# Performance work log

Hardware: AMD Instinct MI355X
Metric: run time of the kernel (lower is better)

## Reference

```python
import jax, jax.numpy as jnp
import numpy as np

N, E, IN, ED, H, C, G, NC = 50000, 800000, 128, 32, 4, 16, 64, 2
HC = H * C  # 64
NEG_SLOPE = 0.2
EPS = 1e-5


def _layernorm(x, g, b):
    mu = jnp.mean(x, axis=-1, keepdims=True)
    var = jnp.mean((x - mu) ** 2, axis=-1, keepdims=True)
    return (x - mu) * jax.lax.rsqrt(var + EPS) * g + b


def _gat(x, src, dst, edge_attr, W, a_src, a_dst, We, a_edge, b):
    """PyG GATConv (v1) with edge features, concat=True."""
    n = x.shape[0]
    h, c = a_src.shape
    xw = (x @ W).reshape(n, h, c)                       # [N,H,C]
    al_src = jnp.sum(xw * a_src, axis=-1)               # [N,H]
    al_dst = jnp.sum(xw * a_dst, axis=-1)               # [N,H]
    ew = (edge_attr @ We).reshape(-1, h, c)             # [Ef,H,C]
    al_e = jnp.sum(ew * a_edge, axis=-1)                # [Ef,H]
    alpha = al_src[src] + al_dst[dst] + al_e            # [Ef,H]
    alpha = jnp.where(alpha > 0, alpha, NEG_SLOPE * alpha)
    # segment softmax over incoming edges of each dst node
    amax = jax.ops.segment_max(alpha, dst, num_segments=n)
    amax = jnp.where(jnp.isfinite(amax), amax, 0.0)
    ex = jnp.exp(alpha - amax[dst])
    denom = jax.ops.segment_sum(ex, dst, num_segments=n)
    att = ex / (denom[dst] + 1e-16)                     # [Ef,H]
    msg = xw[src] * att[:, :, None]                     # [Ef,H,C]
    out = jax.ops.segment_sum(msg, dst, num_segments=n) # [N,H,C]
    return out.reshape(n, h * c) + b


def setup_inputs() -> dict:
    ks = jax.random.split(jax.random.key(0), 24)
    s = 0.1
    inp = {
        "x": jax.random.normal(ks[0], (N, IN), jnp.float32),
        "edge_attr": jax.random.normal(ks[1], (E, ED), jnp.float32),
        "W1": jax.random.normal(ks[2], (IN, HC), jnp.float32) * s,
        "as1": jax.random.normal(ks[3], (H, C), jnp.float32) * s,
        "ad1": jax.random.normal(ks[4], (H, C), jnp.float32) * s,
        "We1": jax.random.normal(ks[5], (ED, HC), jnp.float32) * s,
        "ae1": jax.random.normal(ks[6], (H, C), jnp.float32) * s,
        "b1": jnp.zeros((HC,), jnp.float32),
        "W2": jax.random.normal(ks[7], (HC, HC), jnp.float32) * s,
        "as2": jax.random.normal(ks[8], (H, C), jnp.float32) * s,
        "ad2": jax.random.normal(ks[9], (H, C), jnp.float32) * s,
        "We2": jax.random.normal(ks[10], (ED, HC), jnp.float32) * s,
        "ae2": jax.random.normal(ks[11], (H, C), jnp.float32) * s,
        "b2": jnp.zeros((HC,), jnp.float32),
        "g1": jnp.ones((HC,), jnp.float32),
        "be1": jnp.zeros((HC,), jnp.float32),
        "fw1": jax.random.normal(ks[12], (HC, 32), jnp.float32) * s,
        "fb1": jnp.zeros((32,), jnp.float32),
        "g2": jnp.ones((32,), jnp.float32),
        "be2": jnp.zeros((32,), jnp.float32),
        "fw2": jax.random.normal(ks[13], (32, NC), jnp.float32) * s,
        "fb2": jnp.zeros((NC,), jnp.float32),
        "edge_index": jax.random.randint(ks[14], (2, E), 0, N, jnp.int64),
        "batch": jnp.sort(jax.random.randint(ks[15], (N,), 0, G, jnp.int64)),
    }
    return inp


def reference(x, edge_attr, W1, as1, ad1, We1, ae1, b1, W2, as2, ad2, We2, ae2,
              b2, g1, be1, fw1, fb1, g2, be2, fw2, fb2, edge_index, batch):
    src, dst = edge_index[0], edge_index[1]
    e = edge_attr.shape[0]
    # add_self_loops with fill_value='mean' (mean of incoming edge_attr per node)
    cnt = jax.ops.segment_sum(jnp.ones((e,), x.dtype), dst, num_segments=N)
    loop_ea = jax.ops.segment_sum(edge_attr, dst, num_segments=N) / jnp.clip(cnt, 1.0)[:, None]
    ar = jnp.arange(N)
    src_f = jnp.concatenate([src, ar])
    dst_f = jnp.concatenate([dst, ar])
    ea_f = jnp.concatenate([edge_attr, loop_ea], axis=0)

    h = _gat(x, src_f, dst_f, ea_f, W1, as1, ad1, We1, ae1, b1)
    h = jax.nn.relu(h)
    h = _layernorm(h, g1, be1)
    h = _gat(h, src_f, dst_f, ea_f, W2, as2, ad2, We2, ae2, b2)
    h = jax.nn.relu(h)
    pooled = jax.ops.segment_max(h, batch, num_segments=G)   # global_max_pool
    pooled = jnp.where(jnp.isfinite(pooled), pooled, 0.0)
    z = pooled @ fw1 + fb1
    z = _layernorm(z, g2, be2)
    z = jax.nn.relu(z)
    # dropout(p=0.4) is identity in eval mode
    z = z @ fw2 + fb2
    return jax.nn.log_softmax(z, axis=1)
```

## Files before the change

### kernel.cpp

```cpp
#include <hip/hip_runtime.h>
#include <math.h>

#define N_NODES 50000
#define N_EDGES 800000
#define IN_DIM 128
#define ED_DIM 32
#define NH 4
#define CH 16
#define HC 64
#define NG 64
#define NCL 2
#define NEG_SLOPE 0.2f
#define LN_EPS 1e-5f
#define NBLK1 196

__global__ void k_ve(const float* __restrict__ We1, const float* __restrict__ ae1,
                     const float* __restrict__ We2, const float* __restrict__ ae2,
                     float* __restrict__ Ve) {
    int t = threadIdx.x;
    int d = t >> 3, k = t & 7;
    int l = k >> 2, h = k & 3;
    const float* We = l ? We2 : We1;
    const float* ae = l ? ae2 : ae1;
    float s = 0.f;
    #pragma unroll
    for (int c = 0; c < CH; ++c) s += We[d * HC + h * CH + c] * ae[h * CH + c];
    Ve[d * 8 + k] = s;
}

__global__ void k_hist(const int* __restrict__ dst, int* __restrict__ cnt,
                       int* __restrict__ rank_e) {
    int e = blockIdx.x * 256 + threadIdx.x;
    if (e < N_EDGES) rank_e[e] = atomicAdd(&cnt[dst[e]], 1);
}

__global__ void k_scan_local(const int* __restrict__ cnt, int* __restrict__ tmp_ex,
                             int* __restrict__ bsum) {
    __shared__ int sd[256];
    int t = threadIdx.x, idx = blockIdx.x * 256 + t;
    int v = (idx < N_NODES) ? cnt[idx] : 0;
    sd[t] = v; __syncthreads();
    for (int off = 1; off < 256; off <<= 1) {
        int add = (t >= off) ? sd[t - off] : 0;
        __syncthreads();
        sd[t] += add;
        __syncthreads();
    }
    if (idx < N_NODES) tmp_ex[idx] = sd[t] - v;
    if (t == 255) bsum[blockIdx.x] = sd[t];
}

__global__ void k_scan_bsums(const int* __restrict__ bsum, int* __restrict__ boff) {
    __shared__ int sd[256];
    int t = threadIdx.x;
    int v = (t < NBLK1) ? bsum[t] : 0;
    sd[t] = v; __syncthreads();
    for (int off = 1; off < 256; off <<= 1) {
        int add = (t >= off) ? sd[t - off] : 0;
        __syncthreads();
        sd[t] += add;
        __syncthreads();
    }
    boff[t] = sd[t] - v;
}

__global__ void k_scan_final(const int* __restrict__ tmp_ex, const int* __restrict__ boff,
                             int* __restrict__ row_start) {
    int idx = blockIdx.x * 256 + threadIdx.x;
    if (idx < N_NODES) row_start[idx] = tmp_ex[idx] + boff[blockIdx.x];
    if (idx == 0) row_start[N_NODES] = N_EDGES;
}

__global__ void k_perm(const int* __restrict__ dst, const int* __restrict__ rank_e,
                       const int* __restrict__ row_start, int* __restrict__ perm_csr) {
    int e = blockIdx.x * 256 + threadIdx.x;
    if (e >= N_EDGES) return;
    int pos = row_start[dst[e]] + rank_e[e];
    perm_csr[pos] = e;
}

__global__ void k_edge(const float* __restrict__ ea, const float* __restrict__ Ve,
                       float* __restrict__ ale8) {
    __shared__ float sVe[ED_DIM * 8];
    int t = threadIdx.x;
    if (t < ED_DIM * 8) sVe[t] = Ve[t];
    __syncthreads();
    int e = blockIdx.x * 256 + t;
    if (e >= N_EDGES) return;
    float a[8];
    #pragma unroll
    for (int k = 0; k < 8; ++k) a[k] = 0.f;
    const float4* er4 = (const float4*)(ea + (long long)e * ED_DIM);
    #pragma unroll
    for (int q = 0; q < ED_DIM / 4; ++q) {
        float4 v = er4[q];
        float ev[4] = {v.x, v.y, v.z, v.w};
        #pragma unroll
        for (int u = 0; u < 4; ++u) {
            #pragma unroll
            for (int k = 0; k < 8; ++k) a[k] += ev[u] * sVe[(q * 4 + u) * 8 + k];
        }
    }
    float4* ap = (float4*)(ale8 + (long long)e * 8);
    ap[0] = make_float4(a[0], a[1], a[2], a[3]);
    ap[1] = make_float4(a[4], a[5], a[6], a[7]);
}

__global__ void k_gather(const int* __restrict__ perm, const int* __restrict__ srcI,
                         const float* __restrict__ ale8, int* __restrict__ src_csr,
                         float4* __restrict__ ale1, float4* __restrict__ ale2) {
    int i = blockIdx.x * 256 + threadIdx.x;
    if (i >= N_EDGES) return;
    int e = perm[i];
    const float4* a = (const float4*)(ale8 + (long long)e * 8);
    float4 a0 = a[0];
    float4 a1 = a[1];
    src_csr[i] = srcI[e];
    ale1[i] = a0;
    ale2[i] = a1;
}

template<int K>
__global__ void k_xw(const float* __restrict__ X, const float* __restrict__ W,
                     const float* __restrict__ AS, const float* __restrict__ AD,
                     float* __restrict__ XW, float* __restrict__ ALS, float* __restrict__ ALD) {
    __shared__ float sW[K * HC];
    __shared__ float sX[16 * K];
    int t = threadIdx.x;
    for (int i = t; i < K * HC; i += 256) sW[i] = W[i];
    int nb = blockIdx.x * 16;
    for (int i = t; i < 16 * K; i += 256) sX[i] = X[(long long)nb * K + i];
    __syncthreads();
    int sub = t >> 6, j = t & 63;
    float acc[4] = {0.f, 0.f, 0.f, 0.f};
    #pragma unroll 8
    for (int k = 0; k < K; ++k) {
        float wv = sW[k * HC + j];
        #pragma unroll
        for (int q = 0; q < 4; ++q) acc[q] += sX[(sub + 4 * q) * K + k] * wv;
    }
    float as_ = AS[j], ad_ = AD[j];
    #pragma unroll
    for (int q = 0; q < 4; ++q) {
        int n = nb + sub + 4 * q;
        XW[(long long)n * HC + j] = acc[q];
        float vs = acc[q] * as_, vd = acc[q] * ad_;
        #pragma unroll
        for (int m = 1; m < 16; m <<= 1) { vs += __shfl_xor(vs, m); vd += __shfl_xor(vd, m); }
        if ((j & 15) == 0) {
            int h = j >> 4;
            ALS[n * 4 + h] = vs; ALD[n * 4 + h] = vd;
        }
    }
}

template<bool DO_LN>
__global__ void k_agg(const int* __restrict__ rs, const int* __restrict__ srcs,
                      const float* __restrict__ ale,
                      const float* __restrict__ ALS, const float* __restrict__ ALD,
                      const float* __restrict__ XW, const float* __restrict__ bias,
                      const float* __restrict__ gam, const float* __restrict__ bet,
                      float* __restrict__ OUT) {
    int n = (blockIdx.x * blockDim.x + threadIdx.x) >> 6;
    if (n >= N_NODES) return;
    int lane = threadIdx.x & 63;
    int h = lane >> 4;
    int e0 = rs[n], e1 = rs[n + 1];
    float adn = ALD[n * 4 + h];
    float acc0 = 0.f, l0 = 0.f, as0 = 0.f;
    float acc1 = 0.f, l1 = 0.f, as1 = 0.f;
    float acc2 = 0.f, l2 = 0.f, as2 = 0.f;
    float acc3 = 0.f, l3 = 0.f, as3 = 0.f;
    int e = e0;
    for (; e + 3 < e1; e += 4) {
        int sA = srcs[e], sB = srcs[e + 1], sC = srcs[e + 2], sD = srcs[e + 3];
        float aeA = ale[(e) * 4 + h];
        float aeB = ale[(e + 1) * 4 + h];
        float aeC = ale[(e + 2) * 4 + h];
        float aeD = ale[(e + 3) * 4 + h];
        float xA = XW[sA * HC + lane];
        float xB = XW[sB * HC + lane];
        float xC = XW[sC * HC + lane];
        float xD = XW[sD * HC + lane];
        float aA = ALS[sA * 4 + h] + adn + aeA;
        float aB = ALS[sB * 4 + h] + adn + aeB;
        float aC = ALS[sC * 4 + h] + adn + aeC;
        float aD = ALS[sD * 4 + h] + adn + aeD;
        aA = aA > 0.f ? aA : NEG_SLOPE * aA;
        aB = aB > 0.f ? aB : NEG_SLOPE * aB;
        aC = aC > 0.f ? aC : NEG_SLOPE * aC;
        aD = aD > 0.f ? aD : NEG_SLOPE * aD;
        float qA = __expf(aA), qB = __expf(aB), qC = __expf(aC), qD = __expf(aD);
        acc0 += qA * xA; l0 += qA; as0 += aeA;
        acc1 += qB * xB; l1 += qB; as1 += aeB;
        acc2 += qC * xC; l2 += qC; as2 += aeC;
        acc3 += qD * xD; l3 += qD; as3 += aeD;
    }
    for (; e < e1; ++e) {
        int sA = srcs[e];
        float aeA = ale[(e) * 4 + h];
        float xA = XW[sA * HC + lane];
        float aA = ALS[sA * 4 + h] + adn + aeA;
        aA = aA > 0.f ? aA : NEG_SLOPE * aA;
        float qA = __expf(aA);
        acc0 += qA * xA; l0 += qA; as0 += aeA;
    }
    int d = e1 - e0;
    float invd = 1.f / (float)(d > 0 ? d : 1);
    float aSelf = ALS[n * 4 + h] + adn + (as0 + as1 + as2 + as3) * invd;
    aSelf = aSelf > 0.f ? aSelf : NEG_SLOPE * aSelf;
    float pS = __expf(aSelf);
    float acc = (acc0 + acc1) + (acc2 + acc3) + pS * XW[n * HC + lane];
    float l = (l0 + l1) + (l2 + l3) + pS;
    float v = acc / (l + 1e-16f) + bias[lane];
    v = fmaxf(v, 0.f);
    if (DO_LN) {
        float s1 = v;
        #pragma unroll
        for (int mm = 1; mm < 64; mm <<= 1) s1 += __shfl_xor(s1, mm);
        float mean = s1 * (1.f / 64.f);
        float dd = v - mean;
        float s2 = dd * dd;
        #pragma unroll
        for (int mm = 1; mm < 64; mm <<= 1) s2 += __shfl_xor(s2, mm);
        float var = s2 * (1.f / 64.f);
        v = dd * rsqrtf(var + LN_EPS) * gam[lane] + bet[lane];
    }
    OUT[(long long)n * HC + lane] = v;
}

__global__ void k_pool(const float* __restrict__ H2, const int* __restrict__ batch,
                       float* __restrict__ pooled) {
    int j = threadIdx.x & 63;
    int r = threadIdx.x >> 6;
    int base = blockIdx.x * 128;
    int gcur = -1; float rm = 0.f;
    for (int n = base + r; n < base + 128 && n < N_NODES; n += 4) {
        int g = batch[n];
        if (g != gcur) {
            if (gcur >= 0) atomicMax((unsigned int*)&pooled[gcur * HC + j], __float_as_uint(rm));
            gcur = g; rm = 0.f;
        }
        rm = fmaxf(rm, H2[(long long)n * HC + j]);
    }
    if (gcur >= 0) atomicMax((unsigned int*)&pooled[gcur * HC + j], __float_as_uint(rm));
}

__global__ void k_head(const float* __restrict__ pooled,
                       const float* __restrict__ fw1, const float* __restrict__ fb1,
                       const float* __restrict__ g2, const float* __restrict__ be2,
                       const float* __restrict__ fw2, const float* __restrict__ fb2,
                       float* __restrict__ out) {
    int g = blockIdx.x;
    int j = threadIdx.x;
    float z = 0.f;
    if (j < 32) {
        for (int k = 0; k < HC; ++k) z += pooled[g * HC + k] * fw1[k * 32 + j];
        z += fb1[j];
    }
    float s1 = (j < 32) ? z : 0.f;
    for (int m = 1; m < 32; m <<= 1) s1 += __shfl_xor(s1, m, 32);
    float mean = s1 * (1.f / 32.f);
    float d = z - mean;
    float s2 = (j < 32) ? d * d : 0.f;
    for (int m = 1; m < 32; m <<= 1) s2 += __shfl_xor(s2, m, 32);
    float var = s2 * (1.f / 32.f);
    float zz = 0.f;
    if (j < 32) {
        zz = d * rsqrtf(var + LN_EPS) * g2[j] + be2[j];
        zz = fmaxf(zz, 0.f);
    }
    float p0 = (j < 32) ? zz * fw2[j * NCL + 0] : 0.f;
    float p1 = (j < 32) ? zz * fw2[j * NCL + 1] : 0.f;
    for (int m = 1; m < 32; m <<= 1) { p0 += __shfl_xor(p0, m, 32); p1 += __shfl_xor(p1, m, 32); }
    if (j == 0) {
        float l0 = p0 + fb2[0], l1 = p1 + fb2[1];
        float mx = fmaxf(l0, l1);
        float ls = mx + logf(__expf(l0 - mx) + __expf(l1 - mx));
        out[g * NCL + 0] = l0 - ls;
        out[g * NCL + 1] = l1 - ls;
    }
}

extern "C" void kernel_launch(void* const* d_in, const int* in_sizes, int n_in,
                              void* d_out, int out_size, void* d_ws, size_t ws_size,
                              hipStream_t stream) {
    const float* x   = (const float*)d_in[0];
    const float* ea  = (const float*)d_in[1];
    const float* W1  = (const float*)d_in[2];
    const float* as1 = (const float*)d_in[3];
    const float* ad1 = (const float*)d_in[4];
    const float* We1 = (const float*)d_in[5];
    const float* ae1 = (const float*)d_in[6];
    const float* b1  = (const float*)d_in[7];
    const float* W2  = (const float*)d_in[8];
    const float* as2 = (const float*)d_in[9];
    const float* ad2 = (const float*)d_in[10];
    const float* We2 = (const float*)d_in[11];
    const float* ae2 = (const float*)d_in[12];
    const float* b2  = (const float*)d_in[13];
    const float* g1  = (const float*)d_in[14];
    const float* be1 = (const float*)d_in[15];
    const float* fw1 = (const float*)d_in[16];
    const float* fb1 = (const float*)d_in[17];
    const float* g2  = (const float*)d_in[18];
    const float* be2 = (const float*)d_in[19];
    const float* fw2 = (const float*)d_in[20];
    const float* fb2 = (const float*)d_in[21];
    const int* eidx  = (const int*)d_in[22];
    const int* batch = (const int*)d_in[23];
    const int* srcI = eidx;
    const int* dstI = eidx + N_EDGES;

    char* w = (char*)d_ws;
    auto alloc = [&](size_t bytes) { char* p = w; w += (bytes + 255) & ~(size_t)255; return p; };
    int*   cnt       = (int*)  alloc((size_t)N_NODES * 4);
    int*   row_start = (int*)  alloc((size_t)(N_NODES + 1) * 4);
    int*   rank_e    = (int*)  alloc((size_t)N_EDGES * 4);
    int*   tmp_ex    = (int*)  alloc((size_t)N_NODES * 4);
    int*   bsum      = (int*)  alloc(256 * 4);
    int*   boff      = (int*)  alloc(256 * 4);
    float* Ve        = (float*)alloc(ED_DIM * 8 * 4);
    int*   perm_csr  = (int*)  alloc((size_t)N_EDGES * 4);
    int*   src_csr   = (int*)  alloc((size_t)N_EDGES * 4);
    float* ale8      = (float*)alloc((size_t)N_EDGES * 8 * 4);
    float4* ale1     = (float4*)alloc((size_t)N_EDGES * 16);
    float4* ale2     = (float4*)alloc((size_t)N_EDGES * 16);
    float* xw1       = (float*)alloc((size_t)N_NODES * HC * 4);
    float* als1      = (float*)alloc((size_t)N_NODES * 4 * 4);
    float* ald1      = (float*)alloc((size_t)N_NODES * 4 * 4);
    float* h1        = (float*)alloc((size_t)N_NODES * HC * 4);
    float* als2      = (float*)alloc((size_t)N_NODES * 4 * 4);
    float* ald2      = (float*)alloc((size_t)N_NODES * 4 * 4);
    float* pooled    = (float*)alloc((size_t)NG * HC * 4);
    float* xw2 = xw1;
    float* h2  = h1;

    hipMemsetAsync(cnt, 0, (size_t)N_NODES * 4, stream);
    hipMemsetAsync(pooled, 0, (size_t)NG * HC * 4, stream);

    k_ve<<<1, 256, 0, stream>>>(We1, ae1, We2, ae2, Ve);
    k_hist<<<N_EDGES / 256, 256, 0, stream>>>(dstI, cnt, rank_e);
    k_scan_local<<<NBLK1, 256, 0, stream>>>(cnt, tmp_ex, bsum);
    k_scan_bsums<<<1, 256, 0, stream>>>(bsum, boff);
    k_scan_final<<<NBLK1, 256, 0, stream>>>(tmp_ex, boff, row_start);
    k_edge<<<N_EDGES / 256, 256, 0, stream>>>(ea, Ve, ale8);
    k_perm<<<N_EDGES / 256, 256, 0, stream>>>(dstI, rank_e, row_start, perm_csr);
    k_gather<<<N_EDGES / 256, 256, 0, stream>>>(perm_csr, srcI, ale8, src_csr, ale1, ale2);

    k_xw<IN_DIM><<<N_NODES / 16, 256, 0, stream>>>(x, W1, as1, ad1, xw1, als1, ald1);
    k_agg<true><<<N_NODES / 4, 256, 0, stream>>>(row_start, src_csr, (const float*)ale1,
                                                 als1, ald1, xw1, b1, g1, be1, h1);
    k_xw<HC><<<N_NODES / 16, 256, 0, stream>>>(h1, W2, as2, ad2, xw2, als2, ald2);
    k_agg<false><<<N_NODES / 4, 256, 0, stream>>>(row_start, src_csr, (const float*)ale2,
                                                  als2, ald2, xw2, b2, nullptr, nullptr, h2);

    k_pool<<<(N_NODES + 127) / 128, 256, 0, stream>>>(h2, batch, pooled);
    k_head<<<NG, 64, 0, stream>>>(pooled, fw1, fb1, g2, be2, fw2, fb2, (float*)d_out);
}
```

Baseline: 466.4 us.

## Fuse edge projection, CSR permutation and gather into one scatter kernel

Folds the per-layer edge attention vector computation into the edge kernel's prologue, which every block now recomputes. Merges the block-sum scan into the final scan kernel by having each block redo the small 196-entry scan. Replaces the perm/ale8/gather sequence with a direct scatter of src index and edge logits to their CSR position. This removes five launches and the ale8/perm_csr intermediate traffic, at the cost of scattered (uncoalesced) writes and redundant per-block recomputation.

Result: no change. 465.1 us (-0.3%).

```diff
diff --git a/kernel.cpp b/kernel.cpp
--- a/kernel.cpp
+++ b/kernel.cpp
@@ -14,20 +14,6 @@
 #define LN_EPS 1e-5f
 #define NBLK1 196
 
-__global__ void k_ve(const float* __restrict__ We1, const float* __restrict__ ae1,
-                     const float* __restrict__ We2, const float* __restrict__ ae2,
-                     float* __restrict__ Ve) {
-    int t = threadIdx.x;
-    int d = t >> 3, k = t & 7;
-    int l = k >> 2, h = k & 3;
-    const float* We = l ? We2 : We1;
-    const float* ae = l ? ae2 : ae1;
-    float s = 0.f;
-    #pragma unroll
-    for (int c = 0; c < CH; ++c) s += We[d * HC + h * CH + c] * ae[h * CH + c];
-    Ve[d * 8 + k] = s;
-}
-
 __global__ void k_hist(const int* __restrict__ dst, int* __restrict__ cnt,
                        int* __restrict__ rank_e) {
     int e = blockIdx.x * 256 + threadIdx.x;
@@ -50,7 +36,8 @@
     if (t == 255) bsum[blockIdx.x] = sd[t];
 }
 
-__global__ void k_scan_bsums(const int* __restrict__ bsum, int* __restrict__ boff) {
+__global__ void k_scan_final(const int* __restrict__ tmp_ex, const int* __restrict__ bsum,
+                             int* __restrict__ row_start) {
     __shared__ int sd[256];
     int t = threadIdx.x;
     int v = (t < NBLK1) ? bsum[t] : 0;
@@ -61,29 +48,31 @@
         sd[t] += add;
         __syncthreads();
     }
-    boff[t] = sd[t] - v;
-}
-
-__global__ void k_scan_final(const int* __restrict__ tmp_ex, const int* __restrict__ boff,
-                             int* __restrict__ row_start) {
-    int idx = blockIdx.x * 256 + threadIdx.x;
-    if (idx < N_NODES) row_start[idx] = tmp_ex[idx] + boff[blockIdx.x];
+    int boff = sd[blockIdx.x] - bsum[blockIdx.x];
+    int idx = blockIdx.x * 256 + t;
+    if (idx < N_NODES) row_start[idx] = tmp_ex[idx] + boff;
     if (idx == 0) row_start[N_NODES] = N_EDGES;
 }
 
-__global__ void k_perm(const int* __restrict__ dst, const int* __restrict__ rank_e,
-                       const int* __restrict__ row_start, int* __restrict__ perm_csr) {
-    int e = blockIdx.x * 256 + threadIdx.x;
-    if (e >= N_EDGES) return;
-    int pos = row_start[dst[e]] + rank_e[e];
-    perm_csr[pos] = e;
-}
-
-__global__ void k_edge(const float* __restrict__ ea, const float* __restrict__ Ve,
-                       float* __restrict__ ale8) {
+__global__ void k_edge_fused(const float* __restrict__ ea,
+                             const float* __restrict__ We1, const float* __restrict__ ae1,
+                             const float* __restrict__ We2, const float* __restrict__ ae2,
+                             const int* __restrict__ dstI, const int* __restrict__ srcI,
+                             const int* __restrict__ rank_e, const int* __restrict__ row_start,
+                             float4* __restrict__ ale1, float4* __restrict__ ale2,
+                             int* __restrict__ src_csr) {
     __shared__ float sVe[ED_DIM * 8];
     int t = threadIdx.x;
-    if (t < ED_DIM * 8) sVe[t] = Ve[t];
+    {
+        int d = t >> 3, k = t & 7;
+        int l = k >> 2, h = k & 3;
+        const float* We = l ? We2 : We1;
+        const float* ae = l ? ae2 : ae1;
+        float s = 0.f;
+        #pragma unroll
+        for (int c = 0; c < CH; ++c) s += We[d * HC + h * CH + c] * ae[h * CH + c];
+        sVe[d * 8 + k] = s;
+    }
     __syncthreads();
     int e = blockIdx.x * 256 + t;
     if (e >= N_EDGES) return;
@@ -101,23 +90,10 @@
             for (int k = 0; k < 8; ++k) a[k] += ev[u] * sVe[(q * 4 + u) * 8 + k];
         }
     }
-    float4* ap = (float4*)(ale8 + (long long)e * 8);
-    ap[0] = make_float4(a[0], a[1], a[2], a[3]);
-    ap[1] = make_float4(a[4], a[5], a[6], a[7]);
-}
-
-__global__ void k_gather(const int* __restrict__ perm, const int* __restrict__ srcI,
-                         const float* __restrict__ ale8, int* __restrict__ src_csr,
-                         float4* __restrict__ ale1, float4* __restrict__ ale2) {
-    int i = blockIdx.x * 256 + threadIdx.x;
-    if (i >= N_EDGES) return;
-    int e = perm[i];
-    const float4* a = (const float4*)(ale8 + (long long)e * 8);
-    float4 a0 = a[0];
-    float4 a1 = a[1];
-    src_csr[i] = srcI[e];
-    ale1[i] = a0;
-    ale2[i] = a1;
+    int pos = row_start[dstI[e]] + rank_e[e];
+    src_csr[pos] = srcI[e];
+    ale1[pos] = make_float4(a[0], a[1], a[2], a[3]);
+    ale2[pos] = make_float4(a[4], a[5], a[6], a[7]);
 }
 
 template<int K>
@@ -319,11 +295,7 @@
     int*   rank_e    = (int*)  alloc((size_t)N_EDGES * 4);
     int*   tmp_ex    = (int*)  alloc((size_t)N_NODES * 4);
     int*   bsum      = (int*)  alloc(256 * 4);
-    int*   boff      = (int*)  alloc(256 * 4);
-    float* Ve        = (float*)alloc(ED_DIM * 8 * 4);
-    int*   perm_csr  = (int*)  alloc((size_t)N_EDGES * 4);
     int*   src_csr   = (int*)  alloc((size_t)N_EDGES * 4);
-    float* ale8      = (float*)alloc((size_t)N_EDGES * 8 * 4);
     float4* ale1     = (float4*)alloc((size_t)N_EDGES * 16);
     float4* ale2     = (float4*)alloc((size_t)N_EDGES * 16);
     float* xw1       = (float*)alloc((size_t)N_NODES * HC * 4);
@@ -339,14 +311,11 @@
     hipMemsetAsync(cnt, 0, (size_t)N_NODES * 4, stream);
     hipMemsetAsync(pooled, 0, (size_t)NG * HC * 4, stream);
 
-    k_ve<<<1, 256, 0, stream>>>(We1, ae1, We2, ae2, Ve);
     k_hist<<<N_EDGES / 256, 256, 0, stream>>>(dstI, cnt, rank_e);
     k_scan_local<<<NBLK1, 256, 0, stream>>>(cnt, tmp_ex, bsum);
-    k_scan_bsums<<<1, 256, 0, stream>>>(bsum, boff);
-    k_scan_final<<<NBLK1, 256, 0, stream>>>(tmp_ex, boff, row_start);
-    k_edge<<<N_EDGES / 256, 256, 0, stream>>>(ea, Ve, ale8);
-    k_perm<<<N_EDGES / 256, 256, 0, stream>>>(dstI, rank_e, row_start, perm_csr);
-    k_gather<<<N_EDGES / 256, 256, 0, stream>>>(perm_csr, srcI, ale8, src_csr, ale1, ale2);
+    k_scan_final<<<NBLK1, 256, 0, stream>>>(tmp_ex, bsum, row_start);
+    k_edge_fused<<<N_EDGES / 256, 256, 0, stream>>>(ea, We1, ae1, We2, ae2, dstI, srcI,
+                                                    rank_e, row_start, ale1, ale2, src_csr);
 
     k_xw<IN_DIM><<<N_NODES / 16, 256, 0, stream>>>(x, W1, as1, ad1, xw1, als1, ald1);
     k_agg<true><<<N_NODES / 4, 256, 0, stream>>>(row_start, src_csr, (const float*)ale1,
```
